# Kernel optimization log

Hardware: AMD Instinct MI355X
Metric: run time of the kernel (lower is better)

The kernel has to match this reference:

```python
import jax, jax.numpy as jnp
import numpy as np

# Model constants (match init_kwargs)
H = 256          # hidden_dim
NH = 4           # num_heads
L = 4            # gnn_layers
T = 4            # transformer_layers
KMAX = 10        # k_max for overlap embedding
MAXD = 32        # MAX_DIST
INC = 119        # in_channels (atom vocab)
ED = 5           # edge_dim (bond vocab)
B = 64           # graphs per batch
M_SUB = 32       # subgraphs per graph (m)
KNODE = 32       # nodes per subgraph (k)
S = B * M_SUB    # total subgraphs = 2048
N = S * KNODE    # flattened nodes = 65536
E = 131072       # intra-subgraph directed edges


def _ln(x, g, b):
    mu = x.mean(-1, keepdims=True)
    var = ((x - mu) ** 2).mean(-1, keepdims=True)
    return (x - mu) * jax.lax.rsqrt(var + 1e-5) * g + b


def setup_inputs() -> dict:
    key = jax.random.key(0)
    ks = iter(jax.random.split(key, 24))
    nk = lambda: next(ks)
    rn = lambda k_, shp: 0.02 * jax.random.normal(k_, shp, dtype=jnp.float32)

    x_ids = jax.random.randint(nk(), (N,), 0, INC)
    edge_ids = jax.random.randint(nk(), (E,), 0, ED)
    # intra-subgraph edges: endpoints stay within each block of KNODE nodes
    eps_per = E // S
    base = jnp.repeat(jnp.arange(S) * KNODE, eps_per)
    src = base + jax.random.randint(nk(), (E,), 0, KNODE)
    dst = base + jax.random.randint(nk(), (E,), 0, KNODE)
    ns = jax.random.randint(nk(), (S, KNODE), 0, 500)
    padm = jax.random.uniform(nk(), (S, KNODE)) < 0.1
    nodes_sampled = jnp.where(padm, -1, ns)
    dist = jax.random.randint(nk(), (N,), 0, MAXD + 1)
    lp = -5.0 * jax.random.uniform(nk(), (S,))

    return {
        'x_ids': x_ids, 'edge_ids': edge_ids, 'src': src, 'dst': dst,
        'nodes_sampled': nodes_sampled, 'dist': dist, 'lp': lp,
        'atom_emb': rn(nk(), (INC, H)), 'bond_emb': rn(nk(), (ED, H)),
        'dist_emb': rn(nk(), (MAXD + 1, H)),
        'logp_W': rn(nk(), (H,)), 'logp_b': jnp.zeros((H,)),
        'gnn_eps': jnp.zeros((L,)),
        'gnn_W1': rn(nk(), (L, H, H)), 'gnn_b1': jnp.zeros((L, H)),
        'gnn_W2': rn(nk(), (L, H, H)), 'gnn_b2': jnp.zeros((L, H)),
        'ln1_g': jnp.ones((T, H)), 'ln1_b': jnp.zeros((T, H)),
        'qkv_W': rn(nk(), (T, H, 3 * H)),
        'out_W': rn(nk(), (T, H, H)), 'out_b': jnp.zeros((T, H)),
        'ln2_g': jnp.ones((T, H)), 'ln2_b': jnp.zeros((T, H)),
        'f1_W': rn(nk(), (T, H, 4 * H)), 'f1_b': jnp.zeros((T, 4 * H)),
        'f2_W': rn(nk(), (T, 4 * H, H)), 'f2_b': jnp.zeros((T, H)),
        'lnout_g': jnp.ones((H,)), 'lnout_b': jnp.zeros((H,)),
        'overlap_emb': rn(nk(), (KMAX + 1,)),
        'ht_alpha': jnp.ones(()),
    }


def reference(x_ids, edge_ids, src, dst, nodes_sampled, dist, lp,
              atom_emb, bond_emb, dist_emb, logp_W, logp_b,
              gnn_eps, gnn_W1, gnn_b1, gnn_W2, gnn_b2,
              ln1_g, ln1_b, qkv_W, out_W, out_b, ln2_g, ln2_b,
              f1_W, f1_b, f2_W, f2_b, lnout_g, lnout_b,
              overlap_emb, ht_alpha):
    # ---- flatten / embed node features ----
    valid = (nodes_sampled >= 0).reshape(N)
    valid_f = valid.astype(jnp.float32)[:, None]
    lp = jnp.where(jnp.isfinite(lp), lp, 0.0)
    sub_batch = jnp.arange(N) // KNODE
    dist_c = jnp.clip(dist, 0, MAXD)
    logp_pe = jax.nn.relu(lp[sub_batch][:, None] * logp_W + logp_b)
    h = (atom_emb[x_ids] + dist_emb[dist_c] + logp_pe) * valid_f  # [N,H]
    e = bond_emb[edge_ids]                                        # [E,H]

    # ---- GINE message passing ----
    for l in range(L):
        msg = jax.nn.relu(h[src] + e)                       # [E,H] gather
        agg = jax.ops.segment_sum(msg, dst, num_segments=N) # [N,H] scatter-add
        z = (1.0 + gnn_eps[l]) * h + agg
        z = jax.nn.relu(z @ gnn_W1[l] + gnn_b1[l])
        h = (z @ gnn_W2[l] + gnn_b2[l]) * valid_f

    # ---- pool roots into [B, m, H] tokens ----
    root = jnp.arange(S) * KNODE
    x = h[root].reshape(B, M_SUB, H)
    lp2 = lp.reshape(B, M_SUB)

    # ---- pairwise subgraph overlap bias ----
    nodes = nodes_sampled.reshape(B, M_SUB, KNODE)
    vmask = nodes >= 0
    # eq[b,i,j,ki,kj]: node ki of subgraph i equals node kj of subgraph j
    eq = nodes[:, :, None, :, None] == nodes[:, None, :, None, :]
    overlap = (eq.any(-1) & vmask[:, :, None, :]).sum(-1)  # [B,m,m]
    lp_c = jnp.clip(lp2, -30.0, 0.0)
    bias = overlap_emb[jnp.clip(overlap, 0, KMAX)] - ht_alpha * lp_c[:, None, :]
    bias = bias[:, None]  # [B,1,m,m], broadcast over heads

    # ---- relative-bias transformer ----
    hd = H // NH
    scale = 1.0 / np.sqrt(hd).astype(np.float32)
    for t in range(T):
        r = _ln(x, ln1_g[t], ln1_b[t])
        q, k_, v = jnp.split(r @ qkv_W[t], 3, axis=-1)
        q = q.reshape(B, M_SUB, NH, hd)
        k_ = k_.reshape(B, M_SUB, NH, hd)
        v = v.reshape(B, M_SUB, NH, hd)
        scores = jnp.einsum('bihd,bjhd->bhij', q, k_) * scale + bias
        attn = jax.nn.softmax(scores, axis=-1)
        o = jnp.einsum('bhij,bjhd->bihd', attn, v).reshape(B, M_SUB, H)
        x = x + o @ out_W[t] + out_b[t]
        r2 = _ln(x, ln2_g[t], ln2_b[t])
        x = x + jax.nn.gelu(r2 @ f1_W[t] + f1_b[t], approximate=False) @ f2_W[t] + f2_b[t]

    x = _ln(x, lnout_g, lnout_b)
    # HT-weighted mean over subgraph tokens
    w = jax.nn.softmax(-lp_c, axis=1)
    return (w[:, :, None] * x).sum(1)  # [B,H]
```

## Files before the change

kernel.cpp:

```cpp
#include <hip/hip_runtime.h>
#include <hip/hip_bf16.h>
#include <math.h>

#define HDIM   256
#define NHEAD  4
#define LLAY   4
#define TLAY   4
#define KMAXC  10
#define MAXD   32
#define BATCH  64
#define MSUB   32
#define KNODE  32
#define SSUB   2048
#define NNODE  65536
#define NEDGE  131072
#define EPSPER 64
#define EDN    5
#define BSTR   264

typedef unsigned short u16;
typedef __attribute__((ext_vector_type(8))) short bf16x8;
typedef __attribute__((ext_vector_type(4))) float f32x4;

__device__ __forceinline__ float us2f(u16 u) {
    union { unsigned int i; float f; } x; x.i = ((unsigned int)u) << 16; return x.f;
}
__device__ __forceinline__ u16 f2us(float v) {
    union { float f; unsigned int i; } x; x.f = v;
    unsigned int u = x.i;
    u += 0x7fffu + ((u >> 16) & 1u);
    return (u16)(u >> 16);
}
__device__ __forceinline__ float finite_or_zero(float v) {
    return (v == v && fabsf(v) <= 3.0e38f) ? v : 0.0f;
}
__device__ __forceinline__ void gll16(const u16* g, u16* l) {
    __builtin_amdgcn_global_load_lds(
        (const __attribute__((address_space(1))) unsigned int*)g,
        (__attribute__((address_space(3))) unsigned int*)l, 16, 0, 0);
}

__global__ __launch_bounds__(256) void k_csr(
    const int* __restrict__ src, const int* __restrict__ dst,
    const int* __restrict__ eid, u16* __restrict__ perm, u16* __restrict__ off)
{
    __shared__ int sL[4][64], dL[4][64], eL[4][64];
    int wave = threadIdx.x >> 6, lane = threadIdx.x & 63;
    int sgi = blockIdx.x * 4 + wave;
    sL[wave][lane] = src[sgi * 64 + lane] - sgi * KNODE;
    dL[wave][lane] = dst[sgi * 64 + lane] - sgi * KNODE;
    eL[wave][lane] = eid[sgi * 64 + lane];
    __syncthreads();
    if (lane < 32) {
        int cnt = 0;
        for (int e = 0; e < 64; ++e) cnt += (dL[wave][e] == lane) ? 1 : 0;
        int incl = cnt;
        #pragma unroll
        for (int d = 1; d < 32; d <<= 1) {
            int v = __shfl_up(incl, d, 64);
            if (lane >= d) incl += v;
        }
        int start = incl - cnt;
        off[sgi * 32 + lane] = (u16)start;
        int pos = start;
        for (int e = 0; e < 64; ++e) {
            if (dL[wave][e] == lane) {
                perm[sgi * 64 + pos] = (u16)((sL[wave][e] << 3) | eL[wave][e]);
                ++pos;
            }
        }
    }
}

__global__ __launch_bounds__(256) void k_wtrans(
    const float* __restrict__ W, u16* __restrict__ WT, int K, int N)
{
    __shared__ float til[32][33];
    int k0 = blockIdx.x * 32, n0 = blockIdx.y * 32, s = blockIdx.z;
    const float* Wb = W + (size_t)s * K * N;
    u16* Tb = WT + (size_t)s * N * K;
    int j = threadIdx.x & 31, i0 = threadIdx.x >> 5;
    #pragma unroll
    for (int it = 0; it < 4; ++it) {
        int i = i0 + it * 8;
        til[i][j] = Wb[(size_t)(k0 + i) * N + n0 + j];
    }
    __syncthreads();
    #pragma unroll
    for (int it = 0; it < 4; ++it) {
        int i = i0 + it * 8;
        Tb[(size_t)(n0 + i) * K + k0 + j] = f2us(til[j][i]);
    }
}

__global__ __launch_bounds__(256, 3) void k_gnn4(
    const int* __restrict__ x_ids, const int* __restrict__ dist,
    const int* __restrict__ nodes, const float* __restrict__ lp,
    const float* __restrict__ atom_emb, const float* __restrict__ dist_emb,
    const float* __restrict__ logp_W, const float* __restrict__ logp_b,
    const u16* __restrict__ perm, const u16* __restrict__ off,
    const float* __restrict__ bond_emb, const float* __restrict__ eps_arr,
    const float* __restrict__ b1a, const float* __restrict__ b2a,
    const u16* __restrict__ W1T, const u16* __restrict__ W2T,
    float* __restrict__ x)
{
    __shared__ __align__(16) unsigned char smem[22144];
    u16*   hz    = (u16*)smem;
    float* bondL = (float*)(smem + 16384);
    u16*   permL = (u16*)(smem + 21760);
    u16*   offL  = (u16*)(smem + 21888);
    float* validL= (float*)(smem + 21952);
    float* epsL  = (float*)(smem + 22080);

    int tid = threadIdx.x, lane = tid & 63, wave = tid >> 6;
    int sg = blockIdx.x, row0 = sg * 32;
    int fr = lane & 15, quad = lane >> 4;

    for (int i = tid; i < EDN * BSTR; i += 256) {
        int r = i / BSTR, c = i - r * BSTR;
        bondL[i] = (c < 256) ? bond_emb[r * 256 + c] : 0.f;
    }
    if (tid < 64) permL[tid] = perm[sg * 64 + tid];
    if (tid < 32) {
        offL[tid] = off[sg * 32 + tid];
        validL[tid] = (nodes[row0 + tid] >= 0) ? 1.0f : 0.0f;
    }
    if (tid < 4) epsL[tid] = eps_arr[tid];

    {
        int m = tid >> 3, t8 = tid & 7;
        int rg = row0 + m;
        float valid = (nodes[rg] >= 0) ? 1.0f : 0.0f;
        float lpv = finite_or_zero(lp[rg >> 5]);
        int dc = dist[rg]; dc = dc < 0 ? 0 : (dc > MAXD ? MAXD : dc);
        int xid = x_ids[rg];
        #pragma unroll
        for (int k = 0; k < 4; ++k) {
            int cc = t8 * 4 + k, c = cc * 8;
            float4 a0 = *reinterpret_cast<const float4*>(atom_emb + xid * 256 + c);
            float4 a1 = *reinterpret_cast<const float4*>(atom_emb + xid * 256 + c + 4);
            float4 d0 = *reinterpret_cast<const float4*>(dist_emb + dc * 256 + c);
            float4 d1 = *reinterpret_cast<const float4*>(dist_emb + dc * 256 + c + 4);
            float4 w0 = *reinterpret_cast<const float4*>(logp_W + c);
            float4 w1 = *reinterpret_cast<const float4*>(logp_W + c + 4);
            float4 p0 = *reinterpret_cast<const float4*>(logp_b + c);
            float4 p1 = *reinterpret_cast<const float4*>(logp_b + c + 4);
            union { bf16x8 v; ushort4 h[2]; } o;
            o.h[0] = (ushort4){
                f2us((a0.x + d0.x + fmaxf(lpv * w0.x + p0.x, 0.f)) * valid),
                f2us((a0.y + d0.y + fmaxf(lpv * w0.y + p0.y, 0.f)) * valid),
                f2us((a0.z + d0.z + fmaxf(lpv * w0.z + p0.z, 0.f)) * valid),
                f2us((a0.w + d0.w + fmaxf(lpv * w0.w + p0.w, 0.f)) * valid) };
            o.h[1] = (ushort4){
                f2us((a1.x + d1.x + fmaxf(lpv * w1.x + p1.x, 0.f)) * valid),
                f2us((a1.y + d1.y + fmaxf(lpv * w1.y + p1.y, 0.f)) * valid),
                f2us((a1.z + d1.z + fmaxf(lpv * w1.z + p1.z, 0.f)) * valid),
                f2us((a1.w + d1.w + fmaxf(lpv * w1.w + p1.w, 0.f)) * valid) };
            *reinterpret_cast<bf16x8*>(hz + m * 256 + ((cc ^ (m & 7)) * 8)) = o.v;
        }
    }
    __syncthreads();

    int rl = tid >> 3, g8 = tid & 7;
    for (int l = 0; l < LLAY; ++l) {
        float ep1 = 1.0f + epsL[l];
        {
            int e0 = offL[rl];
            int e1 = (rl < 31) ? offL[rl + 1] : 64;
            float a[32];
            #pragma unroll
            for (int q = 0; q < 32; ++q) a[q] = 0.f;
            for (int j = e0; j < e1; ++j) {
                int ent = permL[j];
                int sl = ent >> 3, be = ent & 7;
                #pragma unroll
                for (int q = 0; q < 4; ++q) {
                    int cc = q * 8 + g8;
                    union { bf16x8 v; u16 s[8]; } hv;
                    hv.v = *reinterpret_cast<const bf16x8*>(
                        hz + sl * 256 + ((cc ^ (sl & 7)) * 8));
                    const float* bp = bondL + be * BSTR + cc * 8;
                    float4 bo0 = *reinterpret_cast<const float4*>(bp);
                    float4 bo1 = *reinterpret_cast<const float4*>(bp + 4);
                    a[q*8+0] += fmaxf(us2f(hv.s[0]) + bo0.x, 0.f);
                    a[q*8+1] += fmaxf(us2f(hv.s[1]) + bo0.y, 0.f);
                    a[q*8+2] += fmaxf(us2f(hv.s[2]) + bo0.z, 0.f);
                    a[q*8+3] += fmaxf(us2f(hv.s[3]) + bo0.w, 0.f);
                    a[q*8+4] += fmaxf(us2f(hv.s[4]) + bo1.x, 0.f);
                    a[q*8+5] += fmaxf(us2f(hv.s[5]) + bo1.y, 0.f);
                    a[q*8+6] += fmaxf(us2f(hv.s[6]) + bo1.z, 0.f);
                    a[q*8+7] += fmaxf(us2f(hv.s[7]) + bo1.w, 0.f);
                }
            }
            __syncthreads();
            #pragma unroll
            for (int q = 0; q < 4; ++q) {
                int cc = q * 8 + g8;
                u16* ptr = hz + rl * 256 + ((cc ^ (rl & 7)) * 8);
                union { bf16x8 v; u16 s[8]; } hv, ov;
                hv.v = *reinterpret_cast<const bf16x8*>(ptr);
                #pragma unroll
                for (int k = 0; k < 8; ++k)
                    ov.s[k] = f2us(ep1 * us2f(hv.s[k]) + a[q * 8 + k]);
                *reinterpret_cast<bf16x8*>(ptr) = ov.v;
            }
        }
        __syncthreads();

        const u16* W1 = W1T + l * 65536;
        const float* b1 = b1a + l * 256;
        f32x4 acc[4][2];
        #pragma unroll
        for (int i = 0; i < 4; ++i) { acc[i][0] = (f32x4){0,0,0,0}; acc[i][1] = (f32x4){0,0,0,0}; }
        #pragma unroll
        for (int kc = 0; kc < 8; ++kc) {
            bf16x8 bfv[2];
            #pragma unroll
            for (int j = 0; j < 2; ++j) {
                int m = j * 16 + fr;
                bfv[j] = *reinterpret_cast<const bf16x8*>(hz + m * 256 + (((kc * 4 + quad) ^ (m & 7)) * 8));
            }
            #pragma unroll
            for (int i = 0; i < 4; ++i) {
                bf16x8 wf = *reinterpret_cast<const bf16x8*>(
                    W1 + (size_t)(wave * 64 + i * 16 + fr) * 256 + kc * 32 + quad * 8);
                acc[i][0] = __builtin_amdgcn_mfma_f32_16x16x32_bf16(wf, bfv[0], acc[i][0], 0, 0, 0);
                acc[i][1] = __builtin_amdgcn_mfma_f32_16x16x32_bf16(wf, bfv[1], acc[i][1], 0, 0, 0);
            }
        }
        __syncthreads();
        #pragma unroll
        for (int i = 0; i < 4; ++i) {
            int n1b = wave * 64 + i * 16 + quad * 4;
            float4 bb = *reinterpret_cast<const float4*>(b1 + n1b);
            #pragma unroll
            for (int j = 0; j < 2; ++j) {
                int m = j * 16 + fr;
                ushort4 o = { f2us(fmaxf(acc[i][j][0] + bb.x, 0.f)),
                              f2us(fmaxf(acc[i][j][1] + bb.y, 0.f)),
                              f2us(fmaxf(acc[i][j][2] + bb.z, 0.f)),
                              f2us(fmaxf(acc[i][j][3] + bb.w, 0.f)) };
                *reinterpret_cast<ushort4*>(hz + m * 256 + (((n1b >> 3) ^ (m & 7)) * 8) + (n1b & 7)) = o;
            }
        }
        __syncthreads();

        const u16* W2 = W2T + l * 65536;
        const float* b2 = b2a + l * 256;
        #pragma unroll
        for (int i = 0; i < 4; ++i) { acc[i][0] = (f32x4){0,0,0,0}; acc[i][1] = (f32x4){0,0,0,0}; }
        #pragma unroll
        for (int kc = 0; kc < 8; ++kc) {
            bf16x8 bfv[2];
            #pragma unroll
            for (int j = 0; j < 2; ++j) {
                int m = j * 16 + fr;
                bfv[j] = *reinterpret_cast<const bf16x8*>(hz + m * 256 + (((kc * 4 + quad) ^ (m & 7)) * 8));
            }
            #pragma unroll
            for (int i = 0; i < 4; ++i) {
                bf16x8 wf = *reinterpret_cast<const bf16x8*>(
                    W2 + (size_t)(wave * 64 + i * 16 + fr) * 256 + kc * 32 + quad * 8);
                acc[i][0] = __builtin_amdgcn_mfma_f32_16x16x32_bf16(wf, bfv[0], acc[i][0], 0, 0, 0);
                acc[i][1] = __builtin_amdgcn_mfma_f32_16x16x32_bf16(wf, bfv[1], acc[i][1], 0, 0, 0);
            }
        }
        __syncthreads();
        if (l < LLAY - 1) {
            #pragma unroll
            for (int i = 0; i < 4; ++i) {
                int n2b = wave * 64 + i * 16 + quad * 4;
                float4 bb = *reinterpret_cast<const float4*>(b2 + n2b);
                #pragma unroll
                for (int j = 0; j < 2; ++j) {
                    int m = j * 16 + fr;
                    float vm = validL[m];
                    ushort4 o = { f2us((acc[i][j][0] + bb.x) * vm),
                                  f2us((acc[i][j][1] + bb.y) * vm),
                                  f2us((acc[i][j][2] + bb.z) * vm),
                                  f2us((acc[i][j][3] + bb.w) * vm) };
                    *reinterpret_cast<ushort4*>(hz + m * 256 + (((n2b >> 3) ^ (m & 7)) * 8) + (n2b & 7)) = o;
                }
            }
            __syncthreads();
        } else {
            if (fr == 0) {
                float vm = validL[0];
                #pragma unroll
                for (int i = 0; i < 4; ++i) {
                    int n2b = wave * 64 + i * 16 + quad * 4;
                    float4 bb = *reinterpret_cast<const float4*>(b2 + n2b);
                    float4 o = { (acc[i][0][0] + bb.x) * vm, (acc[i][0][1] + bb.y) * vm,
                                 (acc[i][0][2] + bb.z) * vm, (acc[i][0][3] + bb.w) * vm };
                    *reinterpret_cast<float4*>(x + (size_t)sg * 256 + n2b) = o;
                }
            }
        }
    }
}

__global__ __launch_bounds__(1024) void k_bias(
    const int* __restrict__ nodes, const float* __restrict__ lp,
    const float* __restrict__ ovl_emb, const float* __restrict__ alpha_p,
    float* __restrict__ bias)
{
    int b = blockIdx.x, tid = threadIdx.x;
    __shared__ int nd[32][32];
    __shared__ unsigned int bmv[32][17];
    __shared__ float lpc[32];
    __shared__ float emb[16];
    nd[tid >> 5][tid & 31] = nodes[b * 1024 + tid];
    if (tid < 512) bmv[tid >> 4][tid & 15] = 0u;
    if (tid < 32) {
        float l = finite_or_zero(lp[b * 32 + tid]);
        l = l < -30.f ? -30.f : (l > 0.f ? 0.f : l);
        lpc[tid] = l;
    }
    if (tid >= 64 && tid < 64 + KMAXC + 1) emb[tid - 64] = ovl_emb[tid - 64];
    __syncthreads();
    int own = nd[tid >> 5][tid & 31];
    if (own >= 0) atomicOr(&bmv[tid >> 5][own >> 5], 1u << (own & 31));
    __syncthreads();
    int i = tid >> 5, j = tid & 31;
    float alpha = alpha_p[0];
    int cnt = 0;
    #pragma unroll
    for (int k = 0; k < 32; ++k) {
        int nk = nd[i][k];
        if (nk >= 0) cnt += (int)((bmv[j][nk >> 5] >> (nk & 31)) & 1u);
    }
    bias[b * 1024 + tid] = emb[cnt > KMAXC ? KMAXC : cnt] - alpha * lpc[j];
}

__global__ __launch_bounds__(256) void k_gemmA_ln(
    const float* __restrict__ X, const u16* __restrict__ BT,
    const float* __restrict__ ln_g, const float* __restrict__ ln_b,
    const float* __restrict__ bias, u16* __restrict__ C,
    int N, int act)
{
    __shared__ __align__(16) u16 As[32 * 256];
    __shared__ __align__(16) u16 Bs[2][64 * 32];
    int tid = threadIdx.x, lane = tid & 63, wave = tid >> 6;
    int wm = wave >> 1, wn = wave & 1;
    int bm = blockIdx.y * 32, bn = blockIdx.x * 64;
    int fr = lane & 15, quad = lane >> 4;

    int srow = lane >> 2, skq = lane & 3;
    const u16* gB = BT + (size_t)(bn + wave * 16 + srow) * 256
                       + (skq ^ ((srow >> 1) & 3)) * 8;
    gll16(gB, &Bs[0][wave * 512]);

    #pragma unroll
    for (int rr = 0; rr < 8; ++rr) {
        int r = wave * 8 + rr;
        float4 xv = *reinterpret_cast<const float4*>(X + (size_t)(bm + r) * 256 + lane * 4);
        float s = xv.x + xv.y + xv.z + xv.w;
        #pragma unroll
        for (int o2 = 32; o2 > 0; o2 >>= 1) s += __shfl_xor(s, o2);
        float mu = s * (1.0f / 256.0f);
        float d0 = xv.x - mu, d1 = xv.y - mu, d2 = xv.z - mu, d3 = xv.w - mu;
        float sq = d0 * d0 + d1 * d1 + d2 * d2 + d3 * d3;
        #pragma unroll
        for (int o2 = 32; o2 > 0; o2 >>= 1) sq += __shfl_xor(sq, o2);
        float rs = rsqrtf(sq * (1.0f / 256.0f) + 1e-5f);
        int c = lane * 4;
        float4 gv = *reinterpret_cast<const float4*>(ln_g + c);
        float4 bv = *reinterpret_cast<const float4*>(ln_b + c);
        ushort4 o = { f2us(d0 * rs * gv.x + bv.x), f2us(d1 * rs * gv.y + bv.y),
                      f2us(d2 * rs * gv.z + bv.z), f2us(d3 * rs * gv.w + bv.w) };
        *reinterpret_cast<ushort4*>(As + r * 256 + (((lane >> 1) ^ (r & 7)) * 8) + (lane & 1) * 4) = o;
    }
    __syncthreads();

    f32x4 acc[2];
    acc[0] = (f32x4){0,0,0,0}; acc[1] = (f32x4){0,0,0,0};
    for (int kc = 0; kc < 8; ++kc) {
        int buf = kc & 1;
        if (kc < 7) gll16(gB + (kc + 1) * 32, &Bs[buf ^ 1][wave * 512]);
        int am = wm * 16 + fr;
        bf16x8 af = *reinterpret_cast<const bf16x8*>(
            As + am * 256 + (((kc * 4 + quad) ^ (am & 7)) * 8));
        bf16x8 bfr[2];
        #pragma unroll
        for (int j = 0; j < 2; ++j) {
            int br = wn * 32 + j * 16 + fr;
            bfr[j] = *reinterpret_cast<const bf16x8*>(
                &Bs[buf][br * 32 + (quad ^ ((br >> 1) & 3)) * 8]);
        }
        acc[0] = __builtin_amdgcn_mfma_f32_16x16x32_bf16(af, bfr[0], acc[0], 0, 0, 0);
        acc[1] = __builtin_amdgcn_mfma_f32_16x16x32_bf16(af, bfr[1], acc[1], 0, 0, 0);
        __syncthreads();
    }
    int crow0 = bm + wm * 16 + quad * 4;
    int ccol0 = bn + wn * 32 + fr;
    #pragma unroll
    for (int r = 0; r < 4; ++r) {
        int m = crow0 + r;
        #pragma unroll
        for (int j = 0; j < 2; ++j) {
            int n = ccol0 + j * 16;
            float v = acc[j][r];
            if (bias) v += bias[n];
            if (act == 2) v = 0.5f * v * (1.0f + erff(v * 0.70710678118654752f));
            C[(size_t)m * N + n] = f2us(v);
        }
    }
}

__global__ __launch_bounds__(256) void k_gemmB(
    const u16* __restrict__ A, const u16* __restrict__ BT,
    const float* __restrict__ bias, float* __restrict__ Cout,
    const float* __restrict__ resid, int M, int K, int N)
{
    __shared__ __align__(16) u16 As[2][32 * 32];
    __shared__ __align__(16) u16 Bs[2][64 * 32];
    int tid = threadIdx.x, lane = tid & 63, wave = tid >> 6;
    int wm = wave >> 1, wn = wave & 1;
    int bm = blockIdx.y * 32, bn = blockIdx.x * 64;
    int fr = lane & 15, quad = lane >> 4;
    int srow = lane >> 2, skq = lane & 3;
    int koff = (skq ^ ((srow >> 1) & 3)) * 8;
    const u16* gA = A + (size_t)(bm + (wave & 1) * 16 + srow) * K + koff;
    const u16* gB = BT + (size_t)(bn + wave * 16 + srow) * K + koff;
    if (wave < 2) gll16(gA, &As[0][wave * 512]);
    gll16(gB, &Bs[0][wave * 512]);
    f32x4 acc[2];
    acc[0] = (f32x4){0,0,0,0}; acc[1] = (f32x4){0,0,0,0};
    int nit = K >> 5;
    __syncthreads();
    for (int it = 0; it < nit; ++it) {
        int buf = it & 1;
        if (it + 1 < nit) {
            int k0 = (it + 1) * 32;
            if (wave < 2) gll16(gA + k0, &As[buf ^ 1][wave * 512]);
            gll16(gB + k0, &Bs[buf ^ 1][wave * 512]);
        }
        int am = wm * 16 + fr;
        bf16x8 af = *reinterpret_cast<const bf16x8*>(
            &As[buf][am * 32 + (quad ^ ((am >> 1) & 3)) * 8]);
        bf16x8 bfr[2];
        #pragma unroll
        for (int j = 0; j < 2; ++j) {
            int br = wn * 32 + j * 16 + fr;
            bfr[j] = *reinterpret_cast<const bf16x8*>(
                &Bs[buf][br * 32 + (quad ^ ((br >> 1) & 3)) * 8]);
        }
        acc[0] = __builtin_amdgcn_mfma_f32_16x16x32_bf16(af, bfr[0], acc[0], 0, 0, 0);
        acc[1] = __builtin_amdgcn_mfma_f32_16x16x32_bf16(af, bfr[1], acc[1], 0, 0, 0);
        __syncthreads();
    }
    int crow0 = bm + wm * 16 + quad * 4;
    int ccol0 = bn + wn * 32 + fr;
    #pragma unroll
    for (int r = 0; r < 4; ++r) {
        int m = crow0 + r;
        #pragma unroll
        for (int j = 0; j < 2; ++j) {
            int n = ccol0 + j * 16;
            float v = acc[j][r] + bias[n] + resid[(size_t)m * N + n];
            Cout[(size_t)m * N + n] = v;
        }
    }
}

__global__ __launch_bounds__(256) void k_attn(
    const u16* __restrict__ qkv, const float* __restrict__ bias, u16* __restrict__ o)
{
    int b = blockIdx.x >> 2, hh = blockIdx.x & 3;
    __shared__ float qs[32][65], ks[32][65], vs[32][65];
    __shared__ float sc[32][33];
    int tid = threadIdx.x;
    #pragma unroll
    for (int u = 0; u < 8; ++u) {
        int idx = tid + u * 256;
        int i = idx >> 6, d = idx & 63;
        size_t base = (size_t)(b * 32 + i) * 768;
        qs[i][d] = us2f(qkv[base + hh * 64 + d]);
        ks[i][d] = us2f(qkv[base + 256 + hh * 64 + d]);
        vs[i][d] = us2f(qkv[base + 512 + hh * 64 + d]);
    }
    __syncthreads();
    #pragma unroll
    for (int u = 0; u < 4; ++u) {
        int p = tid + u * 256;
        int i = p >> 5, j = p & 31;
        float s = 0.f;
        #pragma unroll
        for (int d = 0; d < 64; ++d) s += qs[i][d] * ks[j][d];
        sc[i][j] = s * 0.125f + bias[b * 1024 + i * 32 + j];
    }
    __syncthreads();
    if (tid < 32) {
        int i = tid;
        float m = -1e30f;
        for (int j = 0; j < 32; ++j) m = fmaxf(m, sc[i][j]);
        float sum = 0.f;
        for (int j = 0; j < 32; ++j) { float e = expf(sc[i][j] - m); sc[i][j] = e; sum += e; }
        float inv = 1.0f / sum;
        for (int j = 0; j < 32; ++j) sc[i][j] *= inv;
    }
    __syncthreads();
    #pragma unroll
    for (int u = 0; u < 8; ++u) {
        int idx = tid + u * 256;
        int i = idx >> 6, d = idx & 63;
        float a = 0.f;
        #pragma unroll
        for (int j = 0; j < 32; ++j) a += sc[i][j] * vs[j][d];
        o[(size_t)(b * 32 + i) * 256 + hh * 64 + d] = f2us(a);
    }
}

__global__ __launch_bounds__(256) void k_fin(
    const float* __restrict__ x, const float* __restrict__ lp,
    const float* __restrict__ lnout_g, const float* __restrict__ lnout_b,
    float* __restrict__ out)
{
    __shared__ __align__(16) float xlnf[32 * 260];
    __shared__ float wfin[32];
    int tid = threadIdx.x, lane = tid & 63, wave = tid >> 6;
    int b = blockIdx.x;
    #pragma unroll
    for (int rr = 0; rr < 8; ++rr) {
        int row = wave * 8 + rr;
        float4 xv = *reinterpret_cast<const float4*>(x + (size_t)(b * 32 + row) * 256 + lane * 4);
        float s = xv.x + xv.y + xv.z + xv.w;
        #pragma unroll
        for (int o2 = 32; o2 > 0; o2 >>= 1) s += __shfl_xor(s, o2);
        float mu = s * (1.0f / 256.0f);
        float d0 = xv.x - mu, d1 = xv.y - mu, d2 = xv.z - mu, d3 = xv.w - mu;
        float sq = d0 * d0 + d1 * d1 + d2 * d2 + d3 * d3;
        #pragma unroll
        for (int o2 = 32; o2 > 0; o2 >>= 1) sq += __shfl_xor(sq, o2);
        float rs = rsqrtf(sq * (1.0f / 256.0f) + 1e-5f);
        int c = lane * 4;
        float4 gv = *reinterpret_cast<const float4*>(lnout_g + c);
        float4 bv = *reinterpret_cast<const float4*>(lnout_b + c);
        float4 o = { d0 * rs * gv.x + bv.x, d1 * rs * gv.y + bv.y,
                     d2 * rs * gv.z + bv.z, d3 * rs * gv.w + bv.w };
        *reinterpret_cast<float4*>(xlnf + row * 260 + c) = o;
    }
    __syncthreads();
    if (tid == 0) {
        float l2[32];
        float m = -1e30f;
        for (int i = 0; i < 32; ++i) {
            float l = finite_or_zero(lp[b * 32 + i]);
            l = l < -30.f ? -30.f : (l > 0.f ? 0.f : l);
            l2[i] = -l;
            m = fmaxf(m, -l);
        }
        float s = 0.f;
        for (int i = 0; i < 32; ++i) { float e = expf(l2[i] - m); wfin[i] = e; s += e; }
        float inv = 1.0f / s;
        for (int i = 0; i < 32; ++i) wfin[i] *= inv;
    }
    __syncthreads();
    float a = 0.f;
    for (int i = 0; i < 32; ++i) a += wfin[i] * xlnf[i * 260 + tid];
    out[(size_t)b * 256 + tid] = a;
}

extern "C" void kernel_launch(void* const* d_in, const int* in_sizes, int n_in,
                              void* d_out, int out_size, void* d_ws, size_t ws_size,
                              hipStream_t stream)
{
    const int*   x_ids    = (const int*)d_in[0];
    const int*   edge_ids = (const int*)d_in[1];
    const int*   srcp     = (const int*)d_in[2];
    const int*   dstp     = (const int*)d_in[3];
    const int*   nodes    = (const int*)d_in[4];
    const int*   dist     = (const int*)d_in[5];
    const float* lp       = (const float*)d_in[6];
    const float* atom_emb = (const float*)d_in[7];
    const float* bond_emb = (const float*)d_in[8];
    const float* dist_emb = (const float*)d_in[9];
    const float* logp_W   = (const float*)d_in[10];
    const float* logp_b   = (const float*)d_in[11];
    const float* gnn_eps  = (const float*)d_in[12];
    const float* gnn_W1   = (const float*)d_in[13];
    const float* gnn_b1   = (const float*)d_in[14];
    const float* gnn_W2   = (const float*)d_in[15];
    const float* gnn_b2   = (const float*)d_in[16];
    const float* ln1_g    = (const float*)d_in[17];
    const float* ln1_b    = (const float*)d_in[18];
    const float* qkv_W    = (const float*)d_in[19];
    const float* out_W    = (const float*)d_in[20];
    const float* out_b    = (const float*)d_in[21];
    const float* ln2_g    = (const float*)d_in[22];
    const float* ln2_b    = (const float*)d_in[23];
    const float* f1_W     = (const float*)d_in[24];
    const float* f1_b     = (const float*)d_in[25];
    const float* f2_W     = (const float*)d_in[26];
    const float* f2_b     = (const float*)d_in[27];
    const float* lnout_g  = (const float*)d_in[28];
    const float* lnout_b  = (const float*)d_in[29];
    const float* ovl_emb  = (const float*)d_in[30];
    const float* alpha    = (const float*)d_in[31];

    char* ws = (char*)d_ws;
    u16*   gW1T  = (u16*)(ws + 100663296ull);
    u16*   gW2T  = (u16*)(ws + 100663296ull + 524288ull);
    u16*   permW = (u16*)(ws + 100663296ull + 1048576ull);
    u16*   offW  = (u16*)(ws + 100663296ull + 1310720ull);
    u16*   qkvT  = (u16*)(ws + 33554432ull);
    u16*   outT  = (u16*)(ws + 33554432ull + 1572864ull);
    u16*   f1T   = (u16*)(ws + 33554432ull + 2097152ull);
    u16*   f2T   = (u16*)(ws + 33554432ull + 4194304ull);
    u16*   ob    = (u16*)(ws + 33554432ull + 6291456ull);
    float* biasb = (float*)(ws + 33554432ull + 7340032ull);
    u16*   qkvb  = (u16*)(ws + 33554432ull + 7602176ull);
    u16*   ffh   = (u16*)(ws + 33554432ull + 10747904ull);
    float* x     = (float*)(ws + 67108864ull);

    k_csr<<<SSUB / 4, 256, 0, stream>>>(srcp, dstp, edge_ids, permW, offW);
    k_wtrans<<<dim3(8, 8, 4), 256, 0, stream>>>(gnn_W1, gW1T, 256, 256);
    k_wtrans<<<dim3(8, 8, 4), 256, 0, stream>>>(gnn_W2, gW2T, 256, 256);
    k_gnn4<<<SSUB, 256, 0, stream>>>(
        x_ids, dist, nodes, lp, atom_emb, dist_emb, logp_W, logp_b,
        permW, offW, bond_emb, gnn_eps, gnn_b1, gnn_b2, gW1T, gW2T, x);
    k_wtrans<<<dim3(8, 24, 4), 256, 0, stream>>>(qkv_W, qkvT, 256, 768);
    k_wtrans<<<dim3(8, 8, 4), 256, 0, stream>>>(out_W, outT, 256, 256);
    k_wtrans<<<dim3(8, 32, 4), 256, 0, stream>>>(f1_W, f1T, 256, 1024);
    k_wtrans<<<dim3(32, 8, 4), 256, 0, stream>>>(f2_W, f2T, 1024, 256);
    k_bias<<<BATCH, 1024, 0, stream>>>(nodes, lp, ovl_emb, alpha, biasb);
    for (int t = 0; t < TLAY; ++t) {
        k_gemmA_ln<<<dim3(12, 64), 256, 0, stream>>>(
            x, qkvT + (size_t)t * 768 * 256, ln1_g + t * 256, ln1_b + t * 256,
            nullptr, qkvb, 768, 0);
        k_attn<<<BATCH * NHEAD, 256, 0, stream>>>(qkvb, biasb, ob);
        k_gemmB<<<dim3(4, 64), 256, 0, stream>>>(
            ob, outT + (size_t)t * 65536, out_b + t * 256, x, x, SSUB, 256, 256);
        k_gemmA_ln<<<dim3(16, 64), 256, 0, stream>>>(
            x, f1T + (size_t)t * 1024 * 256, ln2_g + t * 256, ln2_b + t * 256,
            f1_b + t * 1024, ffh, 1024, 2);
        k_gemmB<<<dim3(4, 64), 256, 0, stream>>>(
            ffh, f2T + (size_t)t * 256 * 1024, f2_b + t * 256, x, x, SSUB, 1024, 256);
    }
    k_fin<<<BATCH, 256, 0, stream>>>(x, lp, lnout_g, lnout_b, (float*)d_out);
}
```

Baseline: 614.0 us.

## Process two subgraphs per GNN block with register-resident weights; full-K panels in GEMMs

The fused GNN kernel now handles two subgraphs (64 rows) per block and preloads each layer's weight fragments into registers once, reusing them across four M-tiles instead of reloading them per k-chunk. Its occupancy hint drops from 3 to 2 blocks and LDS use roughly doubles. The transformer GEMM kernels now load whole 256-wide K panels of A and B into shared memory at once, replacing the double-buffered 32-wide K pipeline and removing the per-iteration barriers. The aim is to cut repeated global weight traffic and synchronization. The cost is higher register pressure, more LDS, and less overlap between loads and MFMA work.

```diff
diff --git a/kernel.cpp b/kernel.cpp
--- a/kernel.cpp
+++ b/kernel.cpp
@@ -93,7 +93,7 @@
     }
 }
 
-__global__ __launch_bounds__(256, 3) void k_gnn4(
+__global__ __launch_bounds__(256, 2) void k_gnn4(
     const int* __restrict__ x_ids, const int* __restrict__ dist,
     const int* __restrict__ nodes, const float* __restrict__ lp,
     const float* __restrict__ atom_emb, const float* __restrict__ dist_emb,
@@ -104,39 +104,39 @@
     const u16* __restrict__ W1T, const u16* __restrict__ W2T,
     float* __restrict__ x)
 {
-    __shared__ __align__(16) unsigned char smem[22144];
+    __shared__ __align__(16) unsigned char smem[38912];
     u16*   hz    = (u16*)smem;
-    float* bondL = (float*)(smem + 16384);
-    u16*   permL = (u16*)(smem + 21760);
-    u16*   offL  = (u16*)(smem + 21888);
-    float* validL= (float*)(smem + 21952);
-    float* epsL  = (float*)(smem + 22080);
+    float* bondL = (float*)(smem + 32768);
+    u16*   permL = (u16*)(smem + 38048);
+    u16*   offL  = (u16*)(smem + 38304);
+    float* validL= (float*)(smem + 38432);
+    float* epsL  = (float*)(smem + 38688);
 
     int tid = threadIdx.x, lane = tid & 63, wave = tid >> 6;
-    int sg = blockIdx.x, row0 = sg * 32;
+    int row0 = blockIdx.x * 64;
     int fr = lane & 15, quad = lane >> 4;
 
     for (int i = tid; i < EDN * BSTR; i += 256) {
         int r = i / BSTR, c = i - r * BSTR;
         bondL[i] = (c < 256) ? bond_emb[r * 256 + c] : 0.f;
     }
-    if (tid < 64) permL[tid] = perm[sg * 64 + tid];
-    if (tid < 32) {
-        offL[tid] = off[sg * 32 + tid];
+    if (tid < 128) permL[tid] = perm[blockIdx.x * 128 + tid];
+    if (tid < 64) {
+        offL[tid] = off[blockIdx.x * 64 + tid];
         validL[tid] = (nodes[row0 + tid] >= 0) ? 1.0f : 0.0f;
     }
     if (tid < 4) epsL[tid] = eps_arr[tid];
 
     {
-        int m = tid >> 3, t8 = tid & 7;
+        int m = tid & 63, qd = tid >> 6;
         int rg = row0 + m;
         float valid = (nodes[rg] >= 0) ? 1.0f : 0.0f;
         float lpv = finite_or_zero(lp[rg >> 5]);
         int dc = dist[rg]; dc = dc < 0 ? 0 : (dc > MAXD ? MAXD : dc);
         int xid = x_ids[rg];
         #pragma unroll
-        for (int k = 0; k < 4; ++k) {
-            int cc = t8 * 4 + k, c = cc * 8;
+        for (int k = 0; k < 8; ++k) {
+            int cc = qd * 8 + k, c = cc * 8;
             float4 a0 = *reinterpret_cast<const float4*>(atom_emb + xid * 256 + c);
             float4 a1 = *reinterpret_cast<const float4*>(atom_emb + xid * 256 + c + 4);
             float4 d0 = *reinterpret_cast<const float4*>(dist_emb + dc * 256 + c);
@@ -164,15 +164,17 @@
     int rl = tid >> 3, g8 = tid & 7;
     for (int l = 0; l < LLAY; ++l) {
         float ep1 = 1.0f + epsL[l];
-        {
-            int e0 = offL[rl];
-            int e1 = (rl < 31) ? offL[rl + 1] : 64;
+        for (int p = 0; p < 2; ++p) {
+            int row = p * 32 + rl;
+            int e0 = offL[p * 32 + rl];
+            int e1 = (rl < 31) ? offL[p * 32 + rl + 1] : 64;
             float a[32];
             #pragma unroll
             for (int q = 0; q < 32; ++q) a[q] = 0.f;
             for (int j = e0; j < e1; ++j) {
-                int ent = permL[j];
-                int sl = ent >> 3, be = ent & 7;
+                int ent = permL[p * 64 + j];
+                int sl = p * 32 + (ent >> 3);
+                int be = ent & 7;
                 #pragma unroll
                 for (int q = 0; q < 4; ++q) {
                     int cc = q * 8 + g8;
@@ -196,7 +198,7 @@
             #pragma unroll
             for (int q = 0; q < 4; ++q) {
                 int cc = q * 8 + g8;
-                u16* ptr = hz + rl * 256 + ((cc ^ (rl & 7)) * 8);
+                u16* ptr = hz + row * 256 + ((cc ^ (row & 7)) * 8);
                 union { bf16x8 v; u16 s[8]; } hv, ov;
                 hv.v = *reinterpret_cast<const bf16x8*>(ptr);
                 #pragma unroll
@@ -209,24 +211,31 @@
 
         const u16* W1 = W1T + l * 65536;
         const float* b1 = b1a + l * 256;
-        f32x4 acc[4][2];
-        #pragma unroll
-        for (int i = 0; i < 4; ++i) { acc[i][0] = (f32x4){0,0,0,0}; acc[i][1] = (f32x4){0,0,0,0}; }
+        bf16x8 wf[4][8];
+        #pragma unroll
+        for (int i = 0; i < 4; ++i)
+            #pragma unroll
+            for (int kc = 0; kc < 8; ++kc)
+                wf[i][kc] = *reinterpret_cast<const bf16x8*>(
+                    W1 + (size_t)(wave * 64 + i * 16 + fr) * 256 + kc * 32 + quad * 8);
+        f32x4 acc[4][4];
+        #pragma unroll
+        for (int i = 0; i < 4; ++i)
+            #pragma unroll
+            for (int j = 0; j < 4; ++j) acc[i][j] = (f32x4){0.f, 0.f, 0.f, 0.f};
         #pragma unroll
         for (int kc = 0; kc < 8; ++kc) {
-            bf16x8 bfv[2];
-            #pragma unroll
-            for (int j = 0; j < 2; ++j) {
+            bf16x8 bfv[4];
+            #pragma unroll
+            for (int j = 0; j < 4; ++j) {
                 int m = j * 16 + fr;
                 bfv[j] = *reinterpret_cast<const bf16x8*>(hz + m * 256 + (((kc * 4 + quad) ^ (m & 7)) * 8));
             }
             #pragma unroll
-            for (int i = 0; i < 4; ++i) {
-                bf16x8 wf = *reinterpret_cast<const bf16x8*>(
-                    W1 + (size_t)(wave * 64 + i * 16 + fr) * 256 + kc * 32 + quad * 8);
-                acc[i][0] = __builtin_amdgcn_mfma_f32_16x16x32_bf16(wf, bfv[0], acc[i][0], 0, 0, 0);
-                acc[i][1] = __builtin_amdgcn_mfma_f32_16x16x32_bf16(wf, bfv[1], acc[i][1], 0, 0, 0);
-            }
+            for (int i = 0; i < 4; ++i)
+                #pragma unroll
+                for (int j = 0; j < 4; ++j)
+                    acc[i][j] = __builtin_amdgcn_mfma_f32_16x16x32_bf16(wf[i][kc], bfv[j], acc[i][j], 0, 0, 0);
         }
         __syncthreads();
         #pragma unroll
@@ -234,7 +243,7 @@
             int n1b = wave * 64 + i * 16 + quad * 4;
             float4 bb = *reinterpret_cast<const float4*>(b1 + n1b);
             #pragma unroll
-            for (int j = 0; j < 2; ++j) {
+            for (int j = 0; j < 4; ++j) {
                 int m = j * 16 + fr;
                 ushort4 o = { f2us(fmaxf(acc[i][j][0] + bb.x, 0.f)),
                               f2us(fmaxf(acc[i][j][1] + bb.y, 0.f)),
@@ -248,31 +257,38 @@
         const u16* W2 = W2T + l * 65536;
         const float* b2 = b2a + l * 256;
         #pragma unroll
-        for (int i = 0; i < 4; ++i) { acc[i][0] = (f32x4){0,0,0,0}; acc[i][1] = (f32x4){0,0,0,0}; }
+        for (int i = 0; i < 4; ++i)
+            #pragma unroll
+            for (int kc = 0; kc < 8; ++kc)
+                wf[i][kc] = *reinterpret_cast<const bf16x8*>(
+                    W2 + (size_t)(wave * 64 + i * 16 + fr) * 256 + kc * 32 + quad * 8);
+        #pragma unroll
+        for (int i = 0; i < 4; ++i)
+            #pragma unroll
+            for (int j = 0; j < 4; ++j) acc[i][j] = (f32x4){0.f, 0.f, 0.f, 0.f};
         #pragma unroll
         for (int kc = 0; kc < 8; ++kc) {
-            bf16x8 bfv[2];
-            #pragma unroll
-            for (int j = 0; j < 2; ++j) {
+            bf16x8 bfv[4];
+            #pragma unroll
+            for (int j = 0; j < 4; ++j) {
                 int m = j * 16 + fr;
                 bfv[j] = *reinterpret_cast<const bf16x8*>(hz + m * 256 + (((kc * 4 + quad) ^ (m & 7)) * 8));
             }
             #pragma unroll
-            for (int i = 0; i < 4; ++i) {
-                bf16x8 wf = *reinterpret_cast<const bf16x8*>(
-                    W2 + (size_t)(wave * 64 + i * 16 + fr) * 256 + kc * 32 + quad * 8);
-                acc[i][0] = __builtin_amdgcn_mfma_f32_16x16x32_bf16(wf, bfv[0], acc[i][0], 0, 0, 0);
-                acc[i][1] = __builtin_amdgcn_mfma_f32_16x16x32_bf16(wf, bfv[1], acc[i][1], 0, 0, 0);
-            }
+            for (int i = 0; i < 4; ++i)
+                #pragma unroll
+                for (int j = 0; j < 4; ++j)
+                    acc[i][j] = __builtin_amdgcn_mfma_f32_16x16x32_bf16(wf[i][kc], bfv[j], acc[i][j], 0, 0, 0);
         }
         __syncthreads();
+
         if (l < LLAY - 1) {
             #pragma unroll
             for (int i = 0; i < 4; ++i) {
                 int n2b = wave * 64 + i * 16 + quad * 4;
                 float4 bb = *reinterpret_cast<const float4*>(b2 + n2b);
                 #pragma unroll
-                for (int j = 0; j < 2; ++j) {
+                for (int j = 0; j < 4; ++j) {
                     int m = j * 16 + fr;
                     float vm = validL[m];
                     ushort4 o = { f2us((acc[i][j][0] + bb.x) * vm),
@@ -285,14 +301,21 @@
             __syncthreads();
         } else {
             if (fr == 0) {
-                float vm = validL[0];
                 #pragma unroll
                 for (int i = 0; i < 4; ++i) {
                     int n2b = wave * 64 + i * 16 + quad * 4;
                     float4 bb = *reinterpret_cast<const float4*>(b2 + n2b);
-                    float4 o = { (acc[i][0][0] + bb.x) * vm, (acc[i][0][1] + bb.y) * vm,
-                                 (acc[i][0][2] + bb.z) * vm, (acc[i][0][3] + bb.w) * vm };
-                    *reinterpret_cast<float4*>(x + (size_t)sg * 256 + n2b) = o;
+                    #pragma unroll
+                    for (int jj = 0; jj < 2; ++jj) {
+                        int j = jj * 2, m = j * 16;
+                        float vm = validL[m];
+                        float4 o = { (acc[i][j][0] + bb.x) * vm,
+                                     (acc[i][j][1] + bb.y) * vm,
+                                     (acc[i][j][2] + bb.z) * vm,
+                                     (acc[i][j][3] + bb.w) * vm };
+                        *reinterpret_cast<float4*>(
+                            x + (size_t)(blockIdx.x * 2 + (m >> 5)) * 256 + n2b) = o;
+                    }
                 }
             }
         }
@@ -339,17 +362,20 @@
     int N, int act)
 {
     __shared__ __align__(16) u16 As[32 * 256];
-    __shared__ __align__(16) u16 Bs[2][64 * 32];
+    __shared__ __align__(16) u16 Bs[64 * 256];
     int tid = threadIdx.x, lane = tid & 63, wave = tid >> 6;
     int wm = wave >> 1, wn = wave & 1;
     int bm = blockIdx.y * 32, bn = blockIdx.x * 64;
     int fr = lane & 15, quad = lane >> 4;
 
-    int srow = lane >> 2, skq = lane & 3;
-    const u16* gB = BT + (size_t)(bn + wave * 16 + srow) * 256
-                       + (skq ^ ((srow >> 1) & 3)) * 8;
-    gll16(gB, &Bs[0][wave * 512]);
-
+    #pragma unroll
+    for (int t = 0; t < 8; ++t) {
+        int v = t * 4 + wave;
+        int r = v * 2 + (lane >> 5);
+        int p = lane & 31;
+        int cc = p ^ (r & 7);
+        gll16(BT + (size_t)(bn + r) * 256 + cc * 8, Bs + v * 512);
+    }
     #pragma unroll
     for (int rr = 0; rr < 8; ++rr) {
         int r = wave * 8 + rr;
@@ -374,9 +400,8 @@
 
     f32x4 acc[2];
     acc[0] = (f32x4){0,0,0,0}; acc[1] = (f32x4){0,0,0,0};
+    #pragma unroll
     for (int kc = 0; kc < 8; ++kc) {
-        int buf = kc & 1;
-        if (kc < 7) gll16(gB + (kc + 1) * 32, &Bs[buf ^ 1][wave * 512]);
         int am = wm * 16 + fr;
         bf16x8 af = *reinterpret_cast<const bf16x8*>(
             As + am * 256 + (((kc * 4 + quad) ^ (am & 7)) * 8));
@@ -385,11 +410,10 @@
         for (int j = 0; j < 2; ++j) {
             int br = wn * 32 + j * 16 + fr;
             bfr[j] = *reinterpret_cast<const bf16x8*>(
-                &Bs[buf][br * 32 + (quad ^ ((br >> 1) & 3)) * 8]);
+                Bs + br * 256 + (((kc * 4 + quad) ^ (br & 7)) * 8));
         }
         acc[0] = __builtin_amdgcn_mfma_f32_16x16x32_bf16(af, bfr[0], acc[0], 0, 0, 0);
         acc[1] = __builtin_amdgcn_mfma_f32_16x16x32_bf16(af, bfr[1], acc[1], 0, 0, 0);
-        __syncthreads();
     }
     int crow0 = bm + wm * 16 + quad * 4;
     int ccol0 = bn + wn * 32 + fr;
@@ -412,42 +436,51 @@
     const float* __restrict__ bias, float* __restrict__ Cout,
     const float* __restrict__ resid, int M, int K, int N)
 {
-    __shared__ __align__(16) u16 As[2][32 * 32];
-    __shared__ __align__(16) u16 Bs[2][64 * 32];
+    __shared__ __align__(16) u16 As[32 * 256];
+    __shared__ __align__(16) u16 Bs[64 * 256];
     int tid = threadIdx.x, lane = tid & 63, wave = tid >> 6;
     int wm = wave >> 1, wn = wave & 1;
     int bm = blockIdx.y * 32, bn = blockIdx.x * 64;
     int fr = lane & 15, quad = lane >> 4;
-    int srow = lane >> 2, skq = lane & 3;
-    int koff = (skq ^ ((srow >> 1) & 3)) * 8;
-    const u16* gA = A + (size_t)(bm + (wave & 1) * 16 + srow) * K + koff;
-    const u16* gB = BT + (size_t)(bn + wave * 16 + srow) * K + koff;
-    if (wave < 2) gll16(gA, &As[0][wave * 512]);
-    gll16(gB, &Bs[0][wave * 512]);
+    int npan = K >> 8;
+
     f32x4 acc[2];
     acc[0] = (f32x4){0,0,0,0}; acc[1] = (f32x4){0,0,0,0};
-    int nit = K >> 5;
-    __syncthreads();
-    for (int it = 0; it < nit; ++it) {
-        int buf = it & 1;
-        if (it + 1 < nit) {
-            int k0 = (it + 1) * 32;
-            if (wave < 2) gll16(gA + k0, &As[buf ^ 1][wave * 512]);
-            gll16(gB + k0, &Bs[buf ^ 1][wave * 512]);
-        }
-        int am = wm * 16 + fr;
-        bf16x8 af = *reinterpret_cast<const bf16x8*>(
-            &As[buf][am * 32 + (quad ^ ((am >> 1) & 3)) * 8]);
-        bf16x8 bfr[2];
-        #pragma unroll
-        for (int j = 0; j < 2; ++j) {
-            int br = wn * 32 + j * 16 + fr;
-            bfr[j] = *reinterpret_cast<const bf16x8*>(
-                &Bs[buf][br * 32 + (quad ^ ((br >> 1) & 3)) * 8]);
-        }
-        acc[0] = __builtin_amdgcn_mfma_f32_16x16x32_bf16(af, bfr[0], acc[0], 0, 0, 0);
-        acc[1] = __builtin_amdgcn_mfma_f32_16x16x32_bf16(af, bfr[1], acc[1], 0, 0, 0);
+    for (int pan = 0; pan < npan; ++pan) {
+        if (pan) __syncthreads();
+        int kbase = pan * 256;
+        #pragma unroll
+        for (int t = 0; t < 4; ++t) {
+            int v = t * 4 + wave;
+            int r = v * 2 + (lane >> 5);
+            int p = lane & 31;
+            int cc = p ^ (r & 7);
+            gll16(A + (size_t)(bm + r) * K + kbase + cc * 8, As + v * 512);
+        }
+        #pragma unroll
+        for (int t = 0; t < 8; ++t) {
+            int v = t * 4 + wave;
+            int r = v * 2 + (lane >> 5);
+            int p = lane & 31;
+            int cc = p ^ (r & 7);
+            gll16(BT + (size_t)(bn + r) * K + kbase + cc * 8, Bs + v * 512);
+        }
         __syncthreads();
+        #pragma unroll
+        for (int kc = 0; kc < 8; ++kc) {
+            int am = wm * 16 + fr;
+            bf16x8 af = *reinterpret_cast<const bf16x8*>(
+                As + am * 256 + (((kc * 4 + quad) ^ (am & 7)) * 8));
+            bf16x8 bfr[2];
+            #pragma unroll
+            for (int j = 0; j < 2; ++j) {
+                int br = wn * 32 + j * 16 + fr;
+                bfr[j] = *reinterpret_cast<const bf16x8*>(
+                    Bs + br * 256 + (((kc * 4 + quad) ^ (br & 7)) * 8));
+            }
+            acc[0] = __builtin_amdgcn_mfma_f32_16x16x32_bf16(af, bfr[0], acc[0], 0, 0, 0);
+            acc[1] = __builtin_amdgcn_mfma_f32_16x16x32_bf16(af, bfr[1], acc[1], 0, 0, 0);
+        }
     }
     int crow0 = bm + wm * 16 + quad * 4;
     int ccol0 = bn + wn * 32 + fr;
@@ -457,8 +490,7 @@
         #pragma unroll
         for (int j = 0; j < 2; ++j) {
             int n = ccol0 + j * 16;
-            float v = acc[j][r] + bias[n] + resid[(size_t)m * N + n];
-            Cout[(size_t)m * N + n] = v;
+            Cout[(size_t)m * N + n] = acc[j][r] + bias[n] + resid[(size_t)m * N + n];
         }
     }
 }
@@ -616,7 +648,7 @@
     k_csr<<<SSUB / 4, 256, 0, stream>>>(srcp, dstp, edge_ids, permW, offW);
     k_wtrans<<<dim3(8, 8, 4), 256, 0, stream>>>(gnn_W1, gW1T, 256, 256);
     k_wtrans<<<dim3(8, 8, 4), 256, 0, stream>>>(gnn_W2, gW2T, 256, 256);
-    k_gnn4<<<SSUB, 256, 0, stream>>>(
+    k_gnn4<<<NNODE / 64, 256, 0, stream>>>(
         x_ids, dist, nodes, lp, atom_emb, dist_emb, logp_W, logp_b,
         permW, offW, bond_emb, gnn_eps, gnn_b1, gnn_b2, gW1T, gW2T, x);
     k_wtrans<<<dim3(8, 24, 4), 256, 0, stream>>>(qkv_W, qkvT, 256, 768);
```

Measured after the change: 525.5 us. 14.4% less time.
